# Kernel optimization log

Hardware: AMD Instinct MI355X
Metric: run time of the kernel (lower is better)

Reference implementation:

```python
import jax, jax.numpy as jnp
import numpy as np

KS = 7       # t_kernel_size
PAD = 3      # t_padding
IN_DIM = 64
D_K = 64
D_V = 64


def setup_inputs() -> dict:
    key = jax.random.key(0)
    ks = jax.random.split(key, 9)
    B, C, T, N = 8, IN_DIM, 128, 207
    scale = 1.0 / np.sqrt(C)
    return {
        "q": jax.random.normal(ks[0], (B, C, T, N), jnp.float32),
        "k": jax.random.normal(ks[1], (B, C, T, N), jnp.float32),
        "v": jax.random.normal(ks[2], (B, C, T, N), jnp.float32),
        "Wq": jax.random.normal(ks[3], (D_K, C), jnp.float32) * scale,
        "bq": jax.random.normal(ks[4], (D_K,), jnp.float32) * 0.01,
        "Wk": jax.random.normal(ks[5], (D_K, C), jnp.float32) * scale,
        "bk": jax.random.normal(ks[6], (D_K,), jnp.float32) * 0.01,
        "Wv": jax.random.normal(ks[7], (D_V, C), jnp.float32) * scale,
        "bv": jax.random.normal(ks[8], (D_V,), jnp.float32) * 0.01,
    }


def reference(q, k, v, Wq, bq, Wk, bk, Wv, bv):
    # 1x1 convs == per-position channel projections
    Q = jnp.einsum('bctn,oc->botn', q, Wq) + bq[None, :, None, None]
    K = jnp.einsum('bctn,oc->botn', k, Wk) + bk[None, :, None, None]
    V = jnp.einsum('bctn,oc->botn', v, Wv) + bv[None, :, None, None]
    # conv_k/conv_v zero-pad the time axis by PAD (padding=(t_padding, 0))
    Kp = jnp.pad(K, ((0, 0), (0, 0), (PAD, PAD), (0, 0)))
    Vp = jnp.pad(V, ((0, 0), (0, 0), (PAD, PAD), (0, 0)))
    T_in = q.shape[2]
    T_out = T_in + 2 * PAD - KS + 1  # stride=1, dilation=1 -> == T_in
    # unfold: sliding windows along time; [B, d, T_out, N, KS]
    Kw = jnp.stack([Kp[:, :, i:i + T_out, :] for i in range(KS)], axis=-1)
    Vw = jnp.stack([Vp[:, :, i:i + T_out, :] for i in range(KS)], axis=-1)
    # side='both': center-crop Q to T_out (offset == 0 here)
    off = (T_in - T_out) // 2
    Qs = Q[:, :, off:T_in - off, :]
    # per-channel windowed attention: scores [B, d, T_out, N, KS]
    scores = Qs[..., None] * Kw
    attn = jax.nn.softmax(scores, axis=-1)
    out = jnp.sum(attn * Vw, axis=-1)  # [B, d_v, T_out, N]
    return out
```

## Files before the change

### kernel.cpp

```cpp
#include <hip/hip_runtime.h>

typedef _Float16 half8 __attribute__((ext_vector_type(8)));
typedef float floatx4 __attribute__((ext_vector_type(4)));
typedef float f32x4 __attribute__((ext_vector_type(4)));
typedef unsigned int uint4v __attribute__((ext_vector_type(4)));

#define B_DIM 8
#define C_DIM 64
#define T_DIM 128
#define N_DIM 207
#define O_DIM 64
#define CSTR  (T_DIM * N_DIM)

__global__ void pack_w(const float* __restrict__ Wq,
                       const float* __restrict__ Wk,
                       const float* __restrict__ Wv,
                       _Float16* __restrict__ ws)
{
    int i = threadIdx.x + blockIdx.x * blockDim.x;
    const int per = O_DIM * C_DIM;
    for (int m = i; m < 3 * per; m += blockDim.x * gridDim.x) {
        int arr = m / per, rem = m % per;
        const float* W = (arr == 0) ? Wq : (arr == 1) ? Wk : Wv;
        ws[m] = (_Float16)W[rem];
    }
}


#define GLDS(gp_, lp_)                                                       \
    __builtin_amdgcn_global_load_lds(                                        \
        (const __attribute__((address_space(1))) void*)(gp_),                \
        (__attribute__((address_space(3))) void*)(lp_), 4, 0, 0)

#define STAGE(tg_, P_)                                                       \
    {                                                                        \
        const int tcl_  = min(max((tg_), 0), T_DIM - 1);                     \
        const int toff_ = tcl_ * N_DIM;                                      \
        _Pragma("unroll")                                                    \
        for (int arr_ = 0; arr_ < 3; ++arr_) {                               \
            const float* ab_ = (arr_ == 0) ? qb2 : (arr_ == 1) ? kb2 : vb2;  \
            _Pragma("unroll")                                                \
            for (int i_ = 0; i_ < 4; ++i_) {                                 \
                GLDS(ab_ + toff_ + col_off[i_],                              \
                     &xls[P_][arr_][wv * 4 + i_][0][0]);                     \
            }                                                                \
        }                                                                    \
    }

#define MKFRAG(P_, arr_, kk_, dst_)                                          \
    {                                                                        \
        const float* ch_ = &xls[P_][arr_][qd * 2 + (kk_) * 8][nq][0];        \
        f32x4 A_ = *(const f32x4*)(ch_);                                     \
        f32x4 B_ = *(const f32x4*)(ch_ + 64);                                \
        uint4v t_;                                                           \
        t_[0] = __builtin_bit_cast(unsigned int, __builtin_amdgcn_cvt_pkrtz(A_[0], A_[1])); \
        t_[1] = __builtin_bit_cast(unsigned int, __builtin_amdgcn_cvt_pkrtz(A_[2], A_[3])); \
        t_[2] = __builtin_bit_cast(unsigned int, __builtin_amdgcn_cvt_pkrtz(B_[0], B_[1])); \
        t_[3] = __builtin_bit_cast(unsigned int, __builtin_amdgcn_cvt_pkrtz(B_[2], B_[3])); \
        dst_ = __builtin_bit_cast(half8, t_);                                \
    }

__global__ __launch_bounds__(256, 3)
void attn_mfma(const float* __restrict__ q,
               const float* __restrict__ k,
               const float* __restrict__ v,
               const float* __restrict__ bq,
               const float* __restrict__ bk,
               const float* __restrict__ bv,
               const _Float16* __restrict__ wpk,
               float* __restrict__ out)
{
    __shared__ __align__(16) float xls[2][3][16][16][4];

    const int tid  = threadIdx.x;
    const int lane = tid & 63;
    const int wv   = tid >> 6;
    const int nq   = lane & 15;
    const int qd   = lane >> 4;

    const int nb = blockIdx.x;
    const int tc = blockIdx.y;
    const int b  = blockIdx.z;

    const int t0 = tc * 16;
    const int o0 = wv * 16;
    const int n0 = nb * 16;

    const int cl   = lane & 3;
    const int nrow = lane >> 2;
    const int n_cl = min(n0 + nrow, N_DIM - 1);
    int col_off[4];
    #pragma unroll
    for (int i = 0; i < 4; ++i)
        col_off[i] = ((wv * 4 + i) * 4 + cl) * CSTR + n_cl;

    const float* qb2 = q + (size_t)b * C_DIM * CSTR;
    const float* kb2 = k + (size_t)b * C_DIM * CSTR;
    const float* vb2 = v + (size_t)b * C_DIM * CSTR;

    half8 af[3][2];
    #pragma unroll
    for (int arr = 0; arr < 3; ++arr)
        #pragma unroll
        for (int kk = 0; kk < 2; ++kk)
            af[arr][kk] = *(const half8*)(wpk + ((size_t)(arr * 64 + o0 + nq) * 64
                                                 + qd * 8 + kk * 32));

    float bq_r[4], bk_r[4], bv_r[4];
    #pragma unroll
    for (int j = 0; j < 4; ++j) {
        const int og = o0 + qd * 4 + j;
        bq_r[j] = bq[og]; bk_r[j] = bk[og]; bv_r[j] = bv[og];
    }

    float Kw[4][7], Vw[4][7], Qd4[4][4];
    #pragma unroll
    for (int j = 0; j < 4; ++j) {
        #pragma unroll
        for (int i = 0; i < 7; ++i) { Kw[j][i] = 0.f; Vw[j][i] = 0.f; }
        #pragma unroll
        for (int i = 0; i < 4; ++i) Qd4[j][i] = 0.f;
    }

    STAGE(t0 - 3, 0);

    for (int r = 0; r < 22; ++r) {
        const int p = r & 1;

        if (r <= 6) { asm volatile("s_waitcnt vmcnt(0)"); }
        else        { asm volatile("s_waitcnt vmcnt(4)"); }
        __builtin_amdgcn_s_barrier();
        __builtin_amdgcn_sched_barrier(0);

        if (r < 21) STAGE(t0 - 2 + r, 1 - p);

        half8 fq0, fq1, fk0, fk1, fv0, fv1;
        MKFRAG(p, 1, 0, fk0);  MKFRAG(p, 1, 1, fk1);
        MKFRAG(p, 2, 0, fv0);  MKFRAG(p, 2, 1, fv1);
        MKFRAG(p, 0, 0, fq0);  MKFRAG(p, 0, 1, fq1);

        floatx4 aq = {0.f, 0.f, 0.f, 0.f};
        floatx4 ak = {0.f, 0.f, 0.f, 0.f};
        floatx4 av = {0.f, 0.f, 0.f, 0.f};
        ak = __builtin_amdgcn_mfma_f32_16x16x32_f16(af[1][0], fk0, ak, 0, 0, 0);
        ak = __builtin_amdgcn_mfma_f32_16x16x32_f16(af[1][1], fk1, ak, 0, 0, 0);
        av = __builtin_amdgcn_mfma_f32_16x16x32_f16(af[2][0], fv0, av, 0, 0, 0);
        av = __builtin_amdgcn_mfma_f32_16x16x32_f16(af[2][1], fv1, av, 0, 0, 0);
        aq = __builtin_amdgcn_mfma_f32_16x16x32_f16(af[0][0], fq0, aq, 0, 0, 0);
        aq = __builtin_amdgcn_mfma_f32_16x16x32_f16(af[0][1], fq1, aq, 0, 0, 0);

        const int  tg   = t0 - 3 + r;
        const bool rowv = (tg >= 0) && (tg < T_DIM);

        #pragma unroll
        for (int j = 0; j < 4; ++j) {
            #pragma unroll
            for (int i = 0; i < 6; ++i) { Kw[j][i] = Kw[j][i + 1]; Vw[j][i] = Vw[j][i + 1]; }
            #pragma unroll
            for (int i = 0; i < 3; ++i) Qd4[j][i] = Qd4[j][i + 1];
            Kw[j][6]  = rowv ? (ak[j] + bk_r[j]) : 0.f;
            Vw[j][6]  = rowv ? (av[j] + bv_r[j]) : 0.f;
            Qd4[j][3] = aq[j] + bq_r[j];
        }

        if (r >= 6) {
            const int to  = t0 + r - 6;
            const int n_g = n0 + nq;
            if (n_g < N_DIM) {
                #pragma unroll
                for (int j = 0; j < 4; ++j) {
                    const float qv = Qd4[j][0] * 1.44269504f;
                    float s[7];
                    #pragma unroll
                    for (int i = 0; i < 7; ++i) s[i] = qv * Kw[j][i];
                    float mx = s[0];
                    #pragma unroll
                    for (int i = 1; i < 7; ++i) mx = fmaxf(mx, s[i]);
                    float den = 0.f, num = 0.f;
                    #pragma unroll
                    for (int i = 0; i < 7; ++i) {
                        float e = exp2f(s[i] - mx);
                        den += e;
                        num = fmaf(e, Vw[j][i], num);
                    }
                    out[((size_t)(b * O_DIM + o0 + qd * 4 + j) * T_DIM + to) * N_DIM + n_g]
                        = num * __builtin_amdgcn_rcpf(den);
                }
            }
        }
    }
}

extern "C" void kernel_launch(void* const* d_in, const int* in_sizes, int n_in,
                              void* d_out, int out_size, void* d_ws, size_t ws_size,
                              hipStream_t stream)
{
    const float* q  = (const float*)d_in[0];
    const float* k  = (const float*)d_in[1];
    const float* v  = (const float*)d_in[2];
    const float* Wq = (const float*)d_in[3];
    const float* bq = (const float*)d_in[4];
    const float* Wk = (const float*)d_in[5];
    const float* bk = (const float*)d_in[6];
    const float* Wv = (const float*)d_in[7];
    const float* bv = (const float*)d_in[8];
    float* o = (float*)d_out;

    _Float16* ws_h = (_Float16*)d_ws;

    hipLaunchKernelGGL(pack_w, dim3(3), dim3(256), 0, stream, Wq, Wk, Wv, ws_h);

    dim3 grid(13, 8, B_DIM);
    dim3 block(256);
    hipLaunchKernelGGL(attn_mfma, grid, block, 0, stream,
                       q, k, v, bq, bk, bv, (const _Float16*)ws_h, o);
}
```

Measured before the change: 271.8 us.

## Triple-buffer LDS staging, fully unroll time loop, and swizzle block mapping

```diff
diff --git a/kernel.cpp b/kernel.cpp
--- a/kernel.cpp
+++ b/kernel.cpp
@@ -60,6 +60,67 @@
         dst_ = __builtin_bit_cast(half8, t_);                                \
     }
 
+#define MFMA16(a_, b_, c_) __builtin_amdgcn_mfma_f32_16x16x32_f16(a_, b_, c_, 0, 0, 0)
+
+#define VMWAIT(N_) asm volatile("s_waitcnt vmcnt(" #N_ ")" ::: "memory")
+
+#define STEP(r_, N_)                                                         \
+    {                                                                        \
+        __builtin_amdgcn_sched_barrier(0);                                   \
+        VMWAIT(N_);                                                          \
+        __builtin_amdgcn_s_barrier();                                        \
+        __builtin_amdgcn_sched_barrier(0);                                   \
+        if ((r_) <= 19) STAGE(t0 - 1 + (r_), ((r_) + 2) % 3)                 \
+        __builtin_amdgcn_sched_barrier(0);                                   \
+        half8 fk0, fk1, fv0, fv1;                                            \
+        MKFRAG((r_) % 3, 1, 0, fk0)  MKFRAG((r_) % 3, 1, 1, fk1)             \
+        MKFRAG((r_) % 3, 2, 0, fv0)  MKFRAG((r_) % 3, 2, 1, fv1)             \
+        floatx4 aq = {0.f, 0.f, 0.f, 0.f};                                   \
+        floatx4 ak = {0.f, 0.f, 0.f, 0.f};                                   \
+        floatx4 av = {0.f, 0.f, 0.f, 0.f};                                   \
+        ak = MFMA16(af[1][0], fk0, ak);  ak = MFMA16(af[1][1], fk1, ak);     \
+        av = MFMA16(af[2][0], fv0, av);  av = MFMA16(af[2][1], fv1, av);     \
+        if ((r_) >= 3 && (r_) <= 18) {                                       \
+            half8 fq0, fq1;                                                  \
+            MKFRAG((r_) % 3, 0, 0, fq0)  MKFRAG((r_) % 3, 0, 1, fq1)         \
+            aq = MFMA16(af[0][0], fq0, aq);  aq = MFMA16(af[0][1], fq1, aq); \
+        }                                                                    \
+        const int  tg_   = t0 - 3 + (r_);                                    \
+        const bool rowv_ = (tg_ >= 0) && (tg_ < T_DIM);                      \
+        _Pragma("unroll")                                                    \
+        for (int j = 0; j < 4; ++j) {                                        \
+            Kw[j][(r_) % 7]  = rowv_ ? (ak[j] + bk_r[j]) : 0.f;              \
+            Vw[j][(r_) % 7]  = rowv_ ? (av[j] + bv_r[j]) : 0.f;              \
+            Qd4[j][(r_) % 4] = aq[j] + bq_r[j];                              \
+        }                                                                    \
+        if ((r_) >= 6) {                                                     \
+            const int to_ = t0 + (r_) - 6;                                   \
+            const int n_g = n0 + nq;                                         \
+            if (n_g < N_DIM) {                                               \
+                _Pragma("unroll")                                            \
+                for (int j = 0; j < 4; ++j) {                                \
+                    const float qv = Qd4[j][((r_) + 1) % 4] * 1.44269504f;   \
+                    float s[7];                                              \
+                    _Pragma("unroll")                                        \
+                    for (int i = 0; i < 7; ++i)                              \
+                        s[i] = qv * Kw[j][((r_) + 1 + i) % 7];               \
+                    float mx = s[0];                                         \
+                    _Pragma("unroll")                                        \
+                    for (int i = 1; i < 7; ++i) mx = fmaxf(mx, s[i]);        \
+                    float den = 0.f, num = 0.f;                              \
+                    _Pragma("unroll")                                        \
+                    for (int i = 0; i < 7; ++i) {                            \
+                        float e = exp2f(s[i] - mx);                          \
+                        den += e;                                            \
+                        num = fmaf(e, Vw[j][((r_) + 1 + i) % 7], num);       \
+                    }                                                        \
+                    out[((size_t)(b * O_DIM + o0 + qd * 4 + j) * T_DIM + to_) * N_DIM + n_g] \
+                        = num * __builtin_amdgcn_rcpf(den);                  \
+                }                                                            \
+            }                                                                \
+        }                                                                    \
+    }
+
 __global__ __launch_bounds__(256, 3)
 void attn_mfma(const float* __restrict__ q,
                const float* __restrict__ k,
@@ -70,7 +131,7 @@
                const _Float16* __restrict__ wpk,
                float* __restrict__ out)
 {
-    __shared__ __align__(16) float xls[2][3][16][16][4];
+    __shared__ __align__(16) float xls[3][3][16][16][4];
 
     const int tid  = threadIdx.x;
     const int lane = tid & 63;
@@ -78,9 +139,11 @@
     const int nq   = lane & 15;
     const int qd   = lane >> 4;
 
-    const int nb = blockIdx.x;
-    const int tc = blockIdx.y;
-    const int b  = blockIdx.z;
+    const int bid = (int)blockIdx.x + 13 * ((int)blockIdx.y + 8 * (int)blockIdx.z);
+    const int swz = (bid & 7) * 104 + (bid >> 3);
+    const int nb  = swz % 13;
+    const int tc  = (swz / 13) & 7;
+    const int b   = swz / 104;
 
     const int t0 = tc * 16;
     const int o0 = wv * 16;
@@ -122,73 +185,15 @@
         for (int i = 0; i < 4; ++i) Qd4[j][i] = 0.f;
     }
 
-    STAGE(t0 - 3, 0);
-
-    for (int r = 0; r < 22; ++r) {
-        const int p = r & 1;
-
-        if (r <= 6) { asm volatile("s_waitcnt vmcnt(0)"); }
-        else        { asm volatile("s_waitcnt vmcnt(4)"); }
-        __builtin_amdgcn_s_barrier();
-        __builtin_amdgcn_sched_barrier(0);
-
-        if (r < 21) STAGE(t0 - 2 + r, 1 - p);
-
-        half8 fq0, fq1, fk0, fk1, fv0, fv1;
-        MKFRAG(p, 1, 0, fk0);  MKFRAG(p, 1, 1, fk1);
-        MKFRAG(p, 2, 0, fv0);  MKFRAG(p, 2, 1, fv1);
-        MKFRAG(p, 0, 0, fq0);  MKFRAG(p, 0, 1, fq1);
-
-        floatx4 aq = {0.f, 0.f, 0.f, 0.f};
-        floatx4 ak = {0.f, 0.f, 0.f, 0.f};
-        floatx4 av = {0.f, 0.f, 0.f, 0.f};
-        ak = __builtin_amdgcn_mfma_f32_16x16x32_f16(af[1][0], fk0, ak, 0, 0, 0);
-        ak = __builtin_amdgcn_mfma_f32_16x16x32_f16(af[1][1], fk1, ak, 0, 0, 0);
-        av = __builtin_amdgcn_mfma_f32_16x16x32_f16(af[2][0], fv0, av, 0, 0, 0);
-        av = __builtin_amdgcn_mfma_f32_16x16x32_f16(af[2][1], fv1, av, 0, 0, 0);
-        aq = __builtin_amdgcn_mfma_f32_16x16x32_f16(af[0][0], fq0, aq, 0, 0, 0);
-        aq = __builtin_amdgcn_mfma_f32_16x16x32_f16(af[0][1], fq1, aq, 0, 0, 0);
-
-        const int  tg   = t0 - 3 + r;
-        const bool rowv = (tg >= 0) && (tg < T_DIM);
-
-        #pragma unroll
-        for (int j = 0; j < 4; ++j) {
-            #pragma unroll
-            for (int i = 0; i < 6; ++i) { Kw[j][i] = Kw[j][i + 1]; Vw[j][i] = Vw[j][i + 1]; }
-            #pragma unroll
-            for (int i = 0; i < 3; ++i) Qd4[j][i] = Qd4[j][i + 1];
-            Kw[j][6]  = rowv ? (ak[j] + bk_r[j]) : 0.f;
-            Vw[j][6]  = rowv ? (av[j] + bv_r[j]) : 0.f;
-            Qd4[j][3] = aq[j] + bq_r[j];
-        }
-
-        if (r >= 6) {
-            const int to  = t0 + r - 6;
-            const int n_g = n0 + nq;
-            if (n_g < N_DIM) {
-                #pragma unroll
-                for (int j = 0; j < 4; ++j) {
-                    const float qv = Qd4[j][0] * 1.44269504f;
-                    float s[7];
-                    #pragma unroll
-                    for (int i = 0; i < 7; ++i) s[i] = qv * Kw[j][i];
-                    float mx = s[0];
-                    #pragma unroll
-                    for (int i = 1; i < 7; ++i) mx = fmaxf(mx, s[i]);
-                    float den = 0.f, num = 0.f;
-                    #pragma unroll
-                    for (int i = 0; i < 7; ++i) {
-                        float e = exp2f(s[i] - mx);
-                        den += e;
-                        num = fmaf(e, Vw[j][i], num);
-                    }
-                    out[((size_t)(b * O_DIM + o0 + qd * 4 + j) * T_DIM + to) * N_DIM + n_g]
-                        = num * __builtin_amdgcn_rcpf(den);
-                }
-            }
-        }
-    }
+    STAGE(t0 - 3, 0)
+    STAGE(t0 - 2, 1)
+
+    STEP( 0, 12)  STEP( 1, 12)  STEP( 2, 12)  STEP( 3, 12)
+    STEP( 4, 12)  STEP( 5, 12)  STEP( 6, 12)  STEP( 7, 16)
+    STEP( 8, 20)  STEP( 9, 20)  STEP(10, 20)  STEP(11, 20)
+    STEP(12, 20)  STEP(13, 20)  STEP(14, 20)  STEP(15, 20)
+    STEP(16, 20)  STEP(17, 20)  STEP(18, 20)  STEP(19, 20)
+    STEP(20, 20)  STEP(21,  8)
 }
 
 extern "C" void kernel_launch(void* const* d_in, const int* in_sizes, int n_in,
```

New measurement: 250.5 us. 7.9% less time.
